# Performance work log

Measured on AMD Instinct MI355X. Metric: run time of the kernel, lower is better.

## Reference

```python
import jax, jax.numpy as jnp
import numpy as np

N = 50000      # nodes
E = 800000     # edges (avg degree 16)
D = 64         # input/hidden dim
OUT = 1        # output head dim
ATT_SLOPE = 0.2   # PyG GATConv leaky_relu slope for attention logits
ACT_SLOPE = 0.01  # nn.LeakyReLU default slope


def _gat_layer(x, src, dst, W, a_src, a_dst, b, n):
    """PyG GATConv, heads=1, concat=True, with self-loops already in src/dst."""
    h = x @ W.T                                   # [n, D]
    logit = jax.nn.leaky_relu(h[src] @ a_src + h[dst] @ a_dst, ATT_SLOPE)  # [e]
    m = jax.ops.segment_max(logit, dst, num_segments=n)                    # per-dst max
    e = jnp.exp(logit - m[dst])
    denom = jax.ops.segment_sum(e, dst, num_segments=n)
    coef = e / denom[dst]                         # softmax over incoming edges
    out = jax.ops.segment_sum(coef[:, None] * h[src], dst, num_segments=n)
    return out + b


def setup_inputs() -> dict:
    key = jax.random.key(0)
    ks = jax.random.split(key, 16)
    s = 1.0 / np.sqrt(D)
    inp = {"x": jax.random.normal(ks[0], (N, D), dtype=jnp.float32)}
    for i in range(3):
        inp[f"W{i}"] = jax.random.normal(ks[1 + 4 * i], (D, D), dtype=jnp.float32) * s
        inp[f"a_src{i}"] = jax.random.normal(ks[2 + 4 * i], (D,), dtype=jnp.float32) * s
        inp[f"a_dst{i}"] = jax.random.normal(ks[3 + 4 * i], (D,), dtype=jnp.float32) * s
        inp[f"b{i}"] = jnp.zeros((D,), dtype=jnp.float32)
    inp["Wout"] = jax.random.normal(ks[13], (OUT, D), dtype=jnp.float32) * s
    inp["bout"] = jnp.zeros((OUT,), dtype=jnp.float32)
    inp["edge_index"] = jax.random.randint(ks[14], (2, E), 0, N, dtype=jnp.int64)
    return inp


def reference(x, W0, a_src0, a_dst0, b0, W1, a_src1, a_dst1, b1,
              W2, a_src2, a_dst2, b2, Wout, bout, edge_index):
    n = x.shape[0]
    loops = jnp.arange(n, dtype=edge_index.dtype)
    src = jnp.concatenate([edge_index[0], loops])  # GATConv add_self_loops=True
    dst = jnp.concatenate([edge_index[1], loops])
    act = lambda v: jax.nn.leaky_relu(v, ACT_SLOPE)
    h = act(_gat_layer(x, src, dst, W0, a_src0, a_dst0, b0, n))
    h = act(_gat_layer(h, src, dst, W1, a_src1, a_dst1, b1, n))
    h = act(_gat_layer(h, src, dst, W2, a_src2, a_dst2, b2, n))
    return h @ Wout.T + bout                       # [n, OUT]
```

## Files before the change

kernel.cpp:

```cpp
#include <hip/hip_runtime.h>
#include <hip/hip_fp16.h>

#define DD 64
#define ATT_SLOPE 0.2f
#define ACT_SLOPE 0.01f
#define GNPB 32
#define RCAP 64
#define PA_CHUNK 2048
#define BSH 9
#define BNODES 512
#define BCAP 10240


__device__ __forceinline__ void gemm_body(
        const float* __restrict__ in, const float* __restrict__ W,
        const float* __restrict__ a_src, const float* __restrict__ a_dst,
        __half* __restrict__ h, float* __restrict__ as_out,
        float* __restrict__ ad_out, int n_nodes, int base, float* xin) {
    int t = threadIdx.x;
    int lane = t & 63;
    int w = t >> 6;
    {
        float4* xin4 = (float4*)xin;
        const float4* src4 = (const float4*)in;
        int lim = n_nodes * (DD / 4);
        #pragma unroll
        for (int i = 0; i < (GNPB * DD / 4) / 256; ++i) {
            int idx = i * 256 + t;
            int gi = base * (DD / 4) + idx;
            xin4[idx] = (gi < lim) ? src4[gi]
                                   : make_float4(0.f, 0.f, 0.f, 0.f);
        }
    }
    __syncthreads();

    int n0 = base + w * 8;
    if (n0 >= n_nodes) return;

    float asl = a_src[lane], adl = a_dst[lane];
    const float* wrow = W + (size_t)lane * 64;
    int rmax = n_nodes - n0; if (rmax > 8) rmax = 8;

    if (rmax == 8) {
        float a[8] = {0.f, 0.f, 0.f, 0.f, 0.f, 0.f, 0.f, 0.f};
        #pragma unroll
        for (int kq = 0; kq < 16; ++kq) {
            float4 wv = *(const float4*)(wrow + kq * 4);
            #pragma unroll
            for (int r = 0; r < 8; ++r) {
                float4 xv = *(const float4*)&xin[(w * 8 + r) * DD + kq * 4];
                a[r] = fmaf(xv.x, wv.x, a[r]); a[r] = fmaf(xv.y, wv.y, a[r]);
                a[r] = fmaf(xv.z, wv.z, a[r]); a[r] = fmaf(xv.w, wv.w, a[r]);
            }
        }
        #pragma unroll
        for (int r = 0; r < 8; ++r)
            h[(size_t)(n0 + r) * 64 + lane] = __float2half(a[r]);
        float s[16];
        #pragma unroll
        for (int r = 0; r < 8; ++r) { s[2 * r] = a[r] * asl; s[2 * r + 1] = a[r] * adl; }
        #pragma unroll
        for (int m = 32; m >= 1; m >>= 1) {
            #pragma unroll
            for (int i = 0; i < 16; ++i) s[i] += __shfl_xor(s[i], m, 64);
        }
        if (lane == 0) {
            #pragma unroll
            for (int r = 0; r < 8; ++r) {
                as_out[n0 + r] = s[2 * r];
                ad_out[n0 + r] = s[2 * r + 1];
            }
        }
    } else {
        for (int r = 0; r < rmax; ++r) {
            int node = n0 + r;
            float acc = 0.f;
            #pragma unroll
            for (int kq = 0; kq < 16; ++kq) {
                float4 wv = *(const float4*)(wrow + kq * 4);
                float4 xv = *(const float4*)&xin[(w * 8 + r) * DD + kq * 4];
                acc = fmaf(xv.x, wv.x, acc); acc = fmaf(xv.y, wv.y, acc);
                acc = fmaf(xv.z, wv.z, acc); acc = fmaf(xv.w, wv.w, acc);
            }
            h[(size_t)node * 64 + lane] = __float2half(acc);
            float s1 = acc * asl, s2 = acc * adl;
            #pragma unroll
            for (int m = 32; m >= 1; m >>= 1) {
                s1 += __shfl_xor(s1, m, 64);
                s2 += __shfl_xor(s2, m, 64);
            }
            if (lane == 0) { as_out[node] = s1; ad_out[node] = s2; }
        }
    }
}

__global__ __launch_bounds__(256) void gemm0_binA_kernel(
        const float* __restrict__ x, const float* __restrict__ W,
        const float* __restrict__ a_src, const float* __restrict__ a_dst,
        __half* __restrict__ h, float* __restrict__ as_out,
        float* __restrict__ ad_out, int n_nodes,
        const int* __restrict__ ei, int E,
        int* __restrict__ bcur, unsigned int* __restrict__ bucket_buf,
        int gemm_blocks) {
    __shared__ float xin[GNPB * DD];
    __shared__ int hist[128];
    __shared__ int gbase[128];
    int bid = blockIdx.x;
    if (bid < gemm_blocks) {
        gemm_body(x, W, a_src, a_dst, h, as_out, ad_out, n_nodes,
                  bid * GNPB, xin);
        return;
    }
    int t = threadIdx.x;
    int base_e = (bid - gemm_blocks) * PA_CHUNK;
    int ET = E + n_nodes;
    if (t < 128) hist[t] = 0;
    __syncthreads();

    unsigned int ent[8];
    short eb[8];
    short ep[8];
    #pragma unroll
    for (int j = 0; j < 8; ++j) {
        int e = base_e + j * 256 + t;
        eb[j] = -1;
        if (e >= ET) continue;
        int s, d;
        if (e < E) { s = ei[e]; d = ei[E + e]; }
        else       { s = e - E; d = s; }
        int b = d >> BSH;
        ent[j] = (unsigned int)s | ((unsigned int)(d & (BNODES - 1)) << 16);
        eb[j] = (short)b;
        ep[j] = (short)atomicAdd(&hist[b], 1);
    }
    __syncthreads();
    if (t < 128) {
        int c = hist[t];
        gbase[t] = (c > 0) ? atomicAdd(&bcur[t], c) : 0;
    }
    __syncthreads();
    #pragma unroll
    for (int j = 0; j < 8; ++j) {
        if (eb[j] < 0) continue;
        int pos = gbase[eb[j]] + ep[j];
        if (pos < BCAP) bucket_buf[(size_t)eb[j] * BCAP + pos] = ent[j];
    }
}

__global__ __launch_bounds__(256) void binB_kernel(
        const unsigned int* __restrict__ bucket_buf, const int* __restrict__ bcur,
        int* __restrict__ counts, unsigned short* __restrict__ col_src,
        int n_nodes) {
    __shared__ int cur[BNODES];
    int b = blockIdx.x, t = threadIdx.x;
    for (int i = t; i < BNODES; i += 256) cur[i] = 0;
    __syncthreads();
    int cnt = bcur[b]; if (cnt > BCAP) cnt = BCAP;
    const unsigned int* buf = bucket_buf + (size_t)b * BCAP;
    for (int i = t; i < cnt; i += 256) {
        unsigned int en = buf[i];
        int s = en & 0xFFFF;
        int dl = en >> 16;
        int pos = atomicAdd(&cur[dl], 1);
        if (pos < RCAP)
            col_src[(((b << BSH) + dl) << 6) + pos] = (unsigned short)s;
    }
    __syncthreads();
    int n0 = b << BSH;
    for (int i = t; i < BNODES; i += 256) {
        int d = n0 + i;
        if (d < n_nodes) counts[d] = cur[i];
    }
}

__global__ __launch_bounds__(256) void gemm_alpha_kernel(
        const float* __restrict__ in, const float* __restrict__ W,
        const float* __restrict__ a_src, const float* __restrict__ a_dst,
        __half* __restrict__ h, float* __restrict__ as_out,
        float* __restrict__ ad_out, int n_nodes) {
    __shared__ float xin[GNPB * DD];
    gemm_body(in, W, a_src, a_dst, h, as_out, ad_out, n_nodes,
              blockIdx.x * GNPB, xin);
}

template <bool FUSE_HEAD>
__global__ __launch_bounds__(256) void aggregate_kernel(
        const int* __restrict__ counts, const unsigned short* __restrict__ col_src,
        const __half* __restrict__ h, const float* __restrict__ as_arr,
        const float* __restrict__ ad_arr, const float* __restrict__ b,
        float* __restrict__ out, const float* __restrict__ Wout,
        const float* __restrict__ bout, int n_nodes) {
    int t = threadIdx.x;
    int w = t >> 6, lane = t & 63;
    int node = blockIdx.x * 4 + w;
    if (node >= n_nodes) return;
    int g = lane >> 3, u = lane & 7;

    int beg = node << 6;
    int cnt = __builtin_amdgcn_readfirstlane(counts[node]);
    if (cnt > RCAP) cnt = RCAP;
    int end = beg + cnt;
    float adn = ad_arr[node];

    float acc[8] = {0.f, 0.f, 0.f, 0.f, 0.f, 0.f, 0.f, 0.f};
    float lsum = 0.f;
    int e = beg + g;

    uint4 rA = {0, 0, 0, 0}, rB = {0, 0, 0, 0};
    float aA = 0.f, aB = 0.f;
    if (e < end) {
        int s = col_src[e];
        aA = as_arr[s];
        rA = *(const uint4*)(h + (size_t)s * 64 + u * 8);
    }
    if (e + 8 < end) {
        int s = col_src[e + 8];
        aB = as_arr[s];
        rB = *(const uint4*)(h + (size_t)s * 64 + u * 8);
    }
    while (e < end) {
        int e2 = e + 16;
        uint4 rC = {0, 0, 0, 0}; float aC = 0.f;
        if (e2 < end) {
            int s = col_src[e2];
            aC = as_arr[s];
            rC = *(const uint4*)(h + (size_t)s * 64 + u * 8);
        }
        float lg = aA + adn;
        lg = (lg >= 0.f) ? lg : ATT_SLOPE * lg;
        float p = __expf(lg);
        lsum += p;
        float2 f0 = __half22float2(*(const __half2*)&rA.x);
        float2 f1 = __half22float2(*(const __half2*)&rA.y);
        float2 f2 = __half22float2(*(const __half2*)&rA.z);
        float2 f3 = __half22float2(*(const __half2*)&rA.w);
        acc[0] = fmaf(p, f0.x, acc[0]); acc[1] = fmaf(p, f0.y, acc[1]);
        acc[2] = fmaf(p, f1.x, acc[2]); acc[3] = fmaf(p, f1.y, acc[3]);
        acc[4] = fmaf(p, f2.x, acc[4]); acc[5] = fmaf(p, f2.y, acc[5]);
        acc[6] = fmaf(p, f3.x, acc[6]); acc[7] = fmaf(p, f3.y, acc[7]);
        rA = rB; aA = aB;
        rB = rC; aB = aC;
        e += 8;
    }
    #pragma unroll
    for (int m = 8; m <= 32; m <<= 1) {
        #pragma unroll
        for (int i = 0; i < 8; ++i) acc[i] += __shfl_xor(acc[i], m, 64);
        lsum += __shfl_xor(lsum, m, 64);
    }
    float inv = 1.f / lsum;
    const float4 b0 = *(const float4*)(b + u * 8);
    const float4 b1 = *(const float4*)(b + u * 8 + 4);
    float o[8];
    o[0] = acc[0] * inv + b0.x; o[1] = acc[1] * inv + b0.y;
    o[2] = acc[2] * inv + b0.z; o[3] = acc[3] * inv + b0.w;
    o[4] = acc[4] * inv + b1.x; o[5] = acc[5] * inv + b1.y;
    o[6] = acc[6] * inv + b1.z; o[7] = acc[7] * inv + b1.w;
    #pragma unroll
    for (int i = 0; i < 8; ++i) o[i] = (o[i] >= 0.f) ? o[i] : ACT_SLOPE * o[i];

    if (FUSE_HEAD) {
        const float4 w0 = *(const float4*)(Wout + u * 8);
        const float4 w1 = *(const float4*)(Wout + u * 8 + 4);
        float pd = o[0] * w0.x + o[1] * w0.y + o[2] * w0.z + o[3] * w0.w
                 + o[4] * w1.x + o[5] * w1.y + o[6] * w1.z + o[7] * w1.w;
        #pragma unroll
        for (int m = 1; m <= 4; m <<= 1) pd += __shfl_xor(pd, m, 64);
        if (lane == 0) out[node] = pd + bout[0];
    } else if (g == 0) {
        float4 v0 = {o[0], o[1], o[2], o[3]};
        float4 v1 = {o[4], o[5], o[6], o[7]};
        *(float4*)(out + (size_t)node * 64 + u * 8) = v0;
        *(float4*)(out + (size_t)node * 64 + u * 8 + 4) = v1;
    }
}


extern "C" void kernel_launch(void* const* d_in, const int* in_sizes, int n_in,
                              void* d_out, int out_size, void* d_ws, size_t ws_size,
                              hipStream_t stream) {
    const float* x     = (const float*)d_in[0];
    const float* W[3]  = {(const float*)d_in[1], (const float*)d_in[5], (const float*)d_in[9]};
    const float* as[3] = {(const float*)d_in[2], (const float*)d_in[6], (const float*)d_in[10]};
    const float* ad[3] = {(const float*)d_in[3], (const float*)d_in[7], (const float*)d_in[11]};
    const float* bv[3] = {(const float*)d_in[4], (const float*)d_in[8], (const float*)d_in[12]};
    const float* Wout  = (const float*)d_in[13];
    const float* bout  = (const float*)d_in[14];
    const int*   ei    = (const int*)d_in[15];

    const int N  = in_sizes[0] / DD;
    const int E  = in_sizes[15] / 2;
    const int ET = E + N;
    const int NBUCK = (N + BNODES - 1) >> BSH;

    char* ws = (char*)d_ws;
    size_t off = 0;
    auto alloc = [&](size_t bytes) {
        void* p = ws + off;
        off = (off + bytes + 255) & ~(size_t)255;
        return p;
    };
    unsigned short* col_src = (unsigned short*)alloc((size_t)N * RCAP * 2);
    int*    counts  = (int*)alloc((size_t)N * 4);
    int*    bcur    = (int*)alloc(512 * 4);
    float*  asA     = (float*)alloc((size_t)N * 4);
    float*  adA     = (float*)alloc((size_t)N * 4);
    float*  asB     = (float*)alloc((size_t)N * 4);
    float*  adB     = (float*)alloc((size_t)N * 4);
    __half* hA      = (__half*)alloc((size_t)N * DD * 2);
    __half* hB      = (__half*)alloc((size_t)N * DD * 2);
    float*  obuf    = (float*)alloc((size_t)N * DD * 4);
    (void)ws_size;

    unsigned int* bucket_buf = (unsigned int*)obuf;

    int gridG = (N + GNPB - 1) / GNPB;
    int nA    = (ET + PA_CHUNK - 1) / PA_CHUNK;
    int grid4 = (N + 3) / 4;

    hipMemsetAsync(bcur, 0, 512 * 4, stream);
    gemm0_binA_kernel<<<gridG + nA, 256, 0, stream>>>(
        x, W[0], as[0], ad[0], hA, asA, adA, N,
        ei, E, bcur, bucket_buf, gridG);
    binB_kernel<<<NBUCK, 256, 0, stream>>>(bucket_buf, bcur, counts, col_src, N);

    aggregate_kernel<false><<<grid4, 256, 0, stream>>>(
        counts, col_src, hA, asA, adA, bv[0], obuf, nullptr, nullptr, N);
    gemm_alpha_kernel<<<gridG, 256, 0, stream>>>(obuf, W[1], as[1], ad[1],
                                                 hB, asB, adB, N);
    aggregate_kernel<false><<<grid4, 256, 0, stream>>>(
        counts, col_src, hB, asB, adB, bv[1], obuf, nullptr, nullptr, N);
    gemm_alpha_kernel<<<gridG, 256, 0, stream>>>(obuf, W[2], as[2], ad[2],
                                                 hA, asA, adA, N);
    aggregate_kernel<true><<<grid4, 256, 0, stream>>>(
        counts, col_src, hA, asA, adA, bv[2], (float*)d_out, Wout, bout, N);
}
```

Before: 257.2 us.

## Fuse aggregation with next layer's GEMM and attention projections

Merges each layer's aggregation kernel with the following layer's linear transform and alpha computation. Each wave now aggregates 8 nodes in turn, stages the activated outputs in shared memory, then computes h_next and the attention scalars directly. This removes the fp32 intermediate buffer round trip and two kernel launches. In exchange each wave handles nodes serially and fewer blocks run, which may reduce the latency hiding available for the gathers.

```diff
diff --git a/kernel.cpp b/kernel.cpp
--- a/kernel.cpp
+++ b/kernel.cpp
@@ -10,7 +10,6 @@
 #define BSH 9
 #define BNODES 512
 #define BCAP 10240
-
 
 __device__ __forceinline__ void gemm_body(
         const float* __restrict__ in, const float* __restrict__ W,
@@ -173,105 +172,165 @@
     }
 }
 
-__global__ __launch_bounds__(256) void gemm_alpha_kernel(
-        const float* __restrict__ in, const float* __restrict__ W,
-        const float* __restrict__ a_src, const float* __restrict__ a_dst,
-        __half* __restrict__ h, float* __restrict__ as_out,
-        float* __restrict__ ad_out, int n_nodes) {
-    __shared__ float xin[GNPB * DD];
-    gemm_body(in, W, a_src, a_dst, h, as_out, ad_out, n_nodes,
-              blockIdx.x * GNPB, xin);
-}
-
-template <bool FUSE_HEAD>
-__global__ __launch_bounds__(256) void aggregate_kernel(
+template <int MODE>
+__global__ __launch_bounds__(256) void agg_gemm_kernel(
         const int* __restrict__ counts, const unsigned short* __restrict__ col_src,
         const __half* __restrict__ h, const float* __restrict__ as_arr,
         const float* __restrict__ ad_arr, const float* __restrict__ b,
-        float* __restrict__ out, const float* __restrict__ Wout,
+        const float* __restrict__ Wn, const float* __restrict__ a_srcn,
+        const float* __restrict__ a_dstn, __half* __restrict__ h_next,
+        float* __restrict__ as_next, float* __restrict__ ad_next,
+        float* __restrict__ head_out, const float* __restrict__ Wout,
         const float* __restrict__ bout, int n_nodes) {
+    __shared__ float osh[32 * DD];
     int t = threadIdx.x;
     int w = t >> 6, lane = t & 63;
-    int node = blockIdx.x * 4 + w;
-    if (node >= n_nodes) return;
     int g = lane >> 3, u = lane & 7;
-
-    int beg = node << 6;
-    int cnt = __builtin_amdgcn_readfirstlane(counts[node]);
-    if (cnt > RCAP) cnt = RCAP;
-    int end = beg + cnt;
-    float adn = ad_arr[node];
-
-    float acc[8] = {0.f, 0.f, 0.f, 0.f, 0.f, 0.f, 0.f, 0.f};
-    float lsum = 0.f;
-    int e = beg + g;
-
-    uint4 rA = {0, 0, 0, 0}, rB = {0, 0, 0, 0};
-    float aA = 0.f, aB = 0.f;
-    if (e < end) {
-        int s = col_src[e];
-        aA = as_arr[s];
-        rA = *(const uint4*)(h + (size_t)s * 64 + u * 8);
-    }
-    if (e + 8 < end) {
-        int s = col_src[e + 8];
-        aB = as_arr[s];
-        rB = *(const uint4*)(h + (size_t)s * 64 + u * 8);
-    }
-    while (e < end) {
-        int e2 = e + 16;
-        uint4 rC = {0, 0, 0, 0}; float aC = 0.f;
-        if (e2 < end) {
-            int s = col_src[e2];
-            aC = as_arr[s];
-            rC = *(const uint4*)(h + (size_t)s * 64 + u * 8);
-        }
-        float lg = aA + adn;
-        lg = (lg >= 0.f) ? lg : ATT_SLOPE * lg;
-        float p = __expf(lg);
-        lsum += p;
-        float2 f0 = __half22float2(*(const __half2*)&rA.x);
-        float2 f1 = __half22float2(*(const __half2*)&rA.y);
-        float2 f2 = __half22float2(*(const __half2*)&rA.z);
-        float2 f3 = __half22float2(*(const __half2*)&rA.w);
-        acc[0] = fmaf(p, f0.x, acc[0]); acc[1] = fmaf(p, f0.y, acc[1]);
-        acc[2] = fmaf(p, f1.x, acc[2]); acc[3] = fmaf(p, f1.y, acc[3]);
-        acc[4] = fmaf(p, f2.x, acc[4]); acc[5] = fmaf(p, f2.y, acc[5]);
-        acc[6] = fmaf(p, f3.x, acc[6]); acc[7] = fmaf(p, f3.y, acc[7]);
-        rA = rB; aA = aB;
-        rB = rC; aB = aC;
-        e += 8;
-    }
-    #pragma unroll
-    for (int m = 8; m <= 32; m <<= 1) {
-        #pragma unroll
-        for (int i = 0; i < 8; ++i) acc[i] += __shfl_xor(acc[i], m, 64);
-        lsum += __shfl_xor(lsum, m, 64);
-    }
-    float inv = 1.f / lsum;
+    int nbase = blockIdx.x * 32 + w * 8;
+    if (nbase >= n_nodes) return;
+    int rmax = n_nodes - nbase; if (rmax > 8) rmax = 8;
+
     const float4 b0 = *(const float4*)(b + u * 8);
     const float4 b1 = *(const float4*)(b + u * 8 + 4);
-    float o[8];
-    o[0] = acc[0] * inv + b0.x; o[1] = acc[1] * inv + b0.y;
-    o[2] = acc[2] * inv + b0.z; o[3] = acc[3] * inv + b0.w;
-    o[4] = acc[4] * inv + b1.x; o[5] = acc[5] * inv + b1.y;
-    o[6] = acc[6] * inv + b1.z; o[7] = acc[7] * inv + b1.w;
-    #pragma unroll
-    for (int i = 0; i < 8; ++i) o[i] = (o[i] >= 0.f) ? o[i] : ACT_SLOPE * o[i];
-
-    if (FUSE_HEAD) {
-        const float4 w0 = *(const float4*)(Wout + u * 8);
-        const float4 w1 = *(const float4*)(Wout + u * 8 + 4);
-        float pd = o[0] * w0.x + o[1] * w0.y + o[2] * w0.z + o[3] * w0.w
-                 + o[4] * w1.x + o[5] * w1.y + o[6] * w1.z + o[7] * w1.w;
-        #pragma unroll
-        for (int m = 1; m <= 4; m <<= 1) pd += __shfl_xor(pd, m, 64);
-        if (lane == 0) out[node] = pd + bout[0];
-    } else if (g == 0) {
-        float4 v0 = {o[0], o[1], o[2], o[3]};
-        float4 v1 = {o[4], o[5], o[6], o[7]};
-        *(float4*)(out + (size_t)node * 64 + u * 8) = v0;
-        *(float4*)(out + (size_t)node * 64 + u * 8 + 4) = v1;
+    float4 hw0, hw1;
+    if (MODE == 1) {
+        hw0 = *(const float4*)(Wout + u * 8);
+        hw1 = *(const float4*)(Wout + u * 8 + 4);
+    }
+
+    for (int r = 0; r < rmax; ++r) {
+        int node = nbase + r;
+        int beg = node << 6;
+        int cnt = __builtin_amdgcn_readfirstlane(counts[node]);
+        if (cnt > RCAP) cnt = RCAP;
+        int end = beg + cnt;
+        float adn = ad_arr[node];
+
+        float acc[8] = {0.f, 0.f, 0.f, 0.f, 0.f, 0.f, 0.f, 0.f};
+        float lsum = 0.f;
+        int e = beg + g;
+
+        uint4 rA = {0, 0, 0, 0}, rB = {0, 0, 0, 0};
+        float aA = 0.f, aB = 0.f;
+        if (e < end) {
+            int s = col_src[e];
+            aA = as_arr[s];
+            rA = *(const uint4*)(h + (size_t)s * 64 + u * 8);
+        }
+        if (e + 8 < end) {
+            int s = col_src[e + 8];
+            aB = as_arr[s];
+            rB = *(const uint4*)(h + (size_t)s * 64 + u * 8);
+        }
+        while (e < end) {
+            int e2 = e + 16;
+            uint4 rC = {0, 0, 0, 0}; float aC = 0.f;
+            if (e2 < end) {
+                int s = col_src[e2];
+                aC = as_arr[s];
+                rC = *(const uint4*)(h + (size_t)s * 64 + u * 8);
+            }
+            float lg = aA + adn;
+            lg = (lg >= 0.f) ? lg : ATT_SLOPE * lg;
+            float p = __expf(lg);
+            lsum += p;
+            float2 f0 = __half22float2(*(const __half2*)&rA.x);
+            float2 f1 = __half22float2(*(const __half2*)&rA.y);
+            float2 f2 = __half22float2(*(const __half2*)&rA.z);
+            float2 f3 = __half22float2(*(const __half2*)&rA.w);
+            acc[0] = fmaf(p, f0.x, acc[0]); acc[1] = fmaf(p, f0.y, acc[1]);
+            acc[2] = fmaf(p, f1.x, acc[2]); acc[3] = fmaf(p, f1.y, acc[3]);
+            acc[4] = fmaf(p, f2.x, acc[4]); acc[5] = fmaf(p, f2.y, acc[5]);
+            acc[6] = fmaf(p, f3.x, acc[6]); acc[7] = fmaf(p, f3.y, acc[7]);
+            rA = rB; aA = aB;
+            rB = rC; aB = aC;
+            e += 8;
+        }
+        #pragma unroll
+        for (int m = 8; m <= 32; m <<= 1) {
+            #pragma unroll
+            for (int i = 0; i < 8; ++i) acc[i] += __shfl_xor(acc[i], m, 64);
+            lsum += __shfl_xor(lsum, m, 64);
+        }
+        float inv = 1.f / lsum;
+        float o[8];
+        o[0] = acc[0] * inv + b0.x; o[1] = acc[1] * inv + b0.y;
+        o[2] = acc[2] * inv + b0.z; o[3] = acc[3] * inv + b0.w;
+        o[4] = acc[4] * inv + b1.x; o[5] = acc[5] * inv + b1.y;
+        o[6] = acc[6] * inv + b1.z; o[7] = acc[7] * inv + b1.w;
+        #pragma unroll
+        for (int i = 0; i < 8; ++i) o[i] = (o[i] >= 0.f) ? o[i] : ACT_SLOPE * o[i];
+
+        if (MODE == 1) {
+            float pd = o[0] * hw0.x + o[1] * hw0.y + o[2] * hw0.z + o[3] * hw0.w
+                     + o[4] * hw1.x + o[5] * hw1.y + o[6] * hw1.z + o[7] * hw1.w;
+            #pragma unroll
+            for (int m = 1; m <= 4; m <<= 1) pd += __shfl_xor(pd, m, 64);
+            if (lane == 0) head_out[node] = pd + bout[0];
+        } else if (g == 0) {
+            float* op = &osh[(w * 8 + r) * DD];
+            float4 v0 = {o[0], o[1], o[2], o[3]};
+            float4 v1 = {o[4], o[5], o[6], o[7]};
+            *(float4*)(op + u * 8) = v0;
+            *(float4*)(op + u * 8 + 4) = v1;
+        }
+    }
+
+    if (MODE == 1) return;
+
+    float asl = a_srcn[lane], adl = a_dstn[lane];
+    const float* wrow = Wn + (size_t)lane * 64;
+
+    if (rmax == 8) {
+        float a[8] = {0.f, 0.f, 0.f, 0.f, 0.f, 0.f, 0.f, 0.f};
+        #pragma unroll
+        for (int kq = 0; kq < 16; ++kq) {
+            float4 wv = *(const float4*)(wrow + kq * 4);
+            #pragma unroll
+            for (int r = 0; r < 8; ++r) {
+                float4 xv = *(const float4*)&osh[(w * 8 + r) * DD + kq * 4];
+                a[r] = fmaf(xv.x, wv.x, a[r]); a[r] = fmaf(xv.y, wv.y, a[r]);
+                a[r] = fmaf(xv.z, wv.z, a[r]); a[r] = fmaf(xv.w, wv.w, a[r]);
+            }
+        }
+        #pragma unroll
+        for (int r = 0; r < 8; ++r)
+            h_next[(size_t)(nbase + r) * 64 + lane] = __float2half(a[r]);
+        float s[16];
+        #pragma unroll
+        for (int r = 0; r < 8; ++r) { s[2 * r] = a[r] * asl; s[2 * r + 1] = a[r] * adl; }
+        #pragma unroll
+        for (int m = 32; m >= 1; m >>= 1) {
+            #pragma unroll
+            for (int i = 0; i < 16; ++i) s[i] += __shfl_xor(s[i], m, 64);
+        }
+        if (lane == 0) {
+            #pragma unroll
+            for (int r = 0; r < 8; ++r) {
+                as_next[nbase + r] = s[2 * r];
+                ad_next[nbase + r] = s[2 * r + 1];
+            }
+        }
+    } else {
+        for (int r = 0; r < rmax; ++r) {
+            int node = nbase + r;
+            float acc2 = 0.f;
+            #pragma unroll
+            for (int kq = 0; kq < 16; ++kq) {
+                float4 wv = *(const float4*)(wrow + kq * 4);
+                float4 xv = *(const float4*)&osh[(w * 8 + r) * DD + kq * 4];
+                acc2 = fmaf(xv.x, wv.x, acc2); acc2 = fmaf(xv.y, wv.y, acc2);
+                acc2 = fmaf(xv.z, wv.z, acc2); acc2 = fmaf(xv.w, wv.w, acc2);
+            }
+            h_next[(size_t)node * 64 + lane] = __float2half(acc2);
+            float s1 = acc2 * asl, s2 = acc2 * adl;
+            #pragma unroll
+            for (int m = 32; m >= 1; m >>= 1) {
+                s1 += __shfl_xor(s1, m, 64);
+                s2 += __shfl_xor(s2, m, 64);
+            }
+            if (lane == 0) { as_next[node] = s1; ad_next[node] = s2; }
+        }
     }
 }
 
@@ -309,14 +368,12 @@
     float*  adB     = (float*)alloc((size_t)N * 4);
     __half* hA      = (__half*)alloc((size_t)N * DD * 2);
     __half* hB      = (__half*)alloc((size_t)N * DD * 2);
-    float*  obuf    = (float*)alloc((size_t)N * DD * 4);
+    unsigned int* bucket_buf = (unsigned int*)alloc((size_t)NBUCK * BCAP * 4);
     (void)ws_size;
 
-    unsigned int* bucket_buf = (unsigned int*)obuf;
-
-    int gridG = (N + GNPB - 1) / GNPB;
-    int nA    = (ET + PA_CHUNK - 1) / PA_CHUNK;
-    int grid4 = (N + 3) / 4;
+    int gridG  = (N + GNPB - 1) / GNPB;
+    int nA     = (ET + PA_CHUNK - 1) / PA_CHUNK;
+    int grid32 = (N + 31) / 32;
 
     hipMemsetAsync(bcur, 0, 512 * 4, stream);
     gemm0_binA_kernel<<<gridG + nA, 256, 0, stream>>>(
@@ -324,14 +381,16 @@
         ei, E, bcur, bucket_buf, gridG);
     binB_kernel<<<NBUCK, 256, 0, stream>>>(bucket_buf, bcur, counts, col_src, N);
 
-    aggregate_kernel<false><<<grid4, 256, 0, stream>>>(
-        counts, col_src, hA, asA, adA, bv[0], obuf, nullptr, nullptr, N);
-    gemm_alpha_kernel<<<gridG, 256, 0, stream>>>(obuf, W[1], as[1], ad[1],
-                                                 hB, asB, adB, N);
-    aggregate_kernel<false><<<grid4, 256, 0, stream>>>(
-        counts, col_src, hB, asB, adB, bv[1], obuf, nullptr, nullptr, N);
-    gemm_alpha_kernel<<<gridG, 256, 0, stream>>>(obuf, W[2], as[2], ad[2],
-                                                 hA, asA, adA, N);
-    aggregate_kernel<true><<<grid4, 256, 0, stream>>>(
-        counts, col_src, hA, asA, adA, bv[2], (float*)d_out, Wout, bout, N);
-}
+    agg_gemm_kernel<0><<<grid32, 256, 0, stream>>>(
+        counts, col_src, hA, asA, adA, bv[0],
+        W[1], as[1], ad[1], hB, asB, adB,
+        nullptr, nullptr, nullptr, N);
+    agg_gemm_kernel<0><<<grid32, 256, 0, stream>>>(
+        counts, col_src, hB, asB, adB, bv[1],
+        W[2], as[2], ad[2], hA, asA, adA,
+        nullptr, nullptr, nullptr, N);
+    agg_gemm_kernel<1><<<grid32, 256, 0, stream>>>(
+        counts, col_src, hA, asA, adA, bv[2],
+        nullptr, nullptr, nullptr, nullptr, nullptr, nullptr,
+        (float*)d_out, Wout, bout, N);
+}
```

New measurement: 268.5 us. +4.4%, slower.
